# Optimization experiments

Hardware: AMD Instinct MI355X
Metric: run time of the kernel (lower is better)

The kernel has to match this reference:

```python
import jax, jax.numpy as jnp
import numpy as np

B, N, T = 2, 512, 4096
D_MODEL, N_MODES, NODE_H, EDGE_H = 128, 32, 128, 256


def _lin(key, d_in, d_out, scale=0.02):
    kw, kb = jax.random.split(key)
    W = jax.random.normal(kw, (d_in, d_out), jnp.float32) * scale
    b = jax.random.normal(kb, (d_out,), jnp.float32) * scale
    return W, b


def setup_inputs() -> dict:
    key = jax.random.key(0)
    ks = jax.random.split(key, 12)
    spikes = jax.random.normal(ks[0], (B, N, T), jnp.float32)
    # temporal FNO spectral weights (init * 0.01 as in torch)
    Wr = jax.random.normal(ks[1], (N_MODES, D_MODEL), jnp.float32) * 0.01
    Wi = jax.random.normal(ks[2], (N_MODES, D_MODEL), jnp.float32) * 0.01
    pw1, pb1 = _lin(ks[3], D_MODEL, D_MODEL)
    pw2, pb2 = _lin(ks[4], D_MODEL, D_MODEL)
    nw1, nb1 = _lin(ks[5], D_MODEL, NODE_H)
    nw2, nb2 = _lin(ks[6], NODE_H, D_MODEL)
    sw, sb = _lin(ks[7], D_MODEL, EDGE_H)
    tw, tb = _lin(ks[8], D_MODEL, EDGE_H)
    ew1, eb1 = _lin(ks[9], 2 * EDGE_H, EDGE_H)
    ew2, eb2 = _lin(ks[10], EDGE_H, EDGE_H // 2)
    ew3, eb3 = _lin(ks[11], EDGE_H // 2, 2)
    alpha = jnp.asarray(1.0, jnp.float32)
    beta = jnp.asarray(0.0, jnp.float32)
    return dict(spikes=spikes, Wr=Wr, Wi=Wi, pw1=pw1, pb1=pb1, pw2=pw2, pb2=pb2,
                nw1=nw1, nb1=nb1, nw2=nw2, nb2=nb2, sw=sw, sb=sb, tw=tw, tb=tb,
                ew1=ew1, eb1=eb1, ew2=ew2, eb2=eb2, ew3=ew3, eb3=eb3,
                alpha=alpha, beta=beta)


def reference(spikes, Wr, Wi, pw1, pb1, pw2, pb2, nw1, nb1, nw2, nb2,
              sw, sb, tw, tb, ew1, eb1, ew2, eb2, ew3, eb3, alpha, beta):
    relu = jax.nn.relu
    # --- TemporalFourierOperator1D ---
    xf = jnp.fft.rfft(spikes, axis=-1)[..., :N_MODES]          # [B,N,K] complex
    xr, xi = xf.real.astype(spikes.dtype), xf.imag.astype(spikes.dtype)
    # broadcast complex multiply: [B,N,K,1] x [K,D] -> [B,N,K,D]
    yr = xr[..., None] * Wr - xi[..., None] * Wi
    yi = xr[..., None] * Wi + xi[..., None] * Wr
    E = jnp.sqrt(yr * yr + yi * yi + 1e-8).mean(axis=2)         # [B,N,D]
    E = relu(E @ pw1 + pb1) @ pw2 + pb2                          # post_mlp
    # --- NodeFeatureNet ---
    H = relu(relu(E @ nw1 + nb1) @ nw2 + nb2)                    # [B,N,D]
    # --- EdgeFourierCoeffNet ---
    hs = H @ sw + sb                                             # [B,N,Eh]
    ht = H @ tw + tb
    # concat([hs,ht]) @ ew1 == hs @ ew1[:Eh] + ht @ ew1[Eh:] (exact same math)
    ps = hs @ ew1[:EDGE_H]                                       # [B,N,Eh]
    pt = ht @ ew1[EDGE_H:]
    h = relu(ps[:, :, None, :] + pt[:, None, :, :] + eb1)        # [B,N,N,Eh]
    h = relu(h @ ew2 + eb2)                                      # [B,N,N,Eh/2]
    rt = h @ ew3 + eb3                                           # [B,N,N,2]
    coeffs = rt[..., 0] + 1j * rt[..., 1]                        # [B,N,N] complex
    # --- AdjacencyLinearDecoder2D ---
    adj_spatial = jnp.fft.ifft2(coeffs, axes=(-2, -1)).real
    adj_logits = alpha * adj_spatial + beta
    adj_prob = jax.nn.sigmoid(adj_logits)
    return adj_logits, adj_prob
```

## Files before the change

### kernel.cpp

```cpp
#include <hip/hip_runtime.h>
#include <hip/hip_bf16.h>
#include <math.h>

typedef __attribute__((ext_vector_type(8))) short short8;
typedef __attribute__((ext_vector_type(8))) _Float16 f16x8;
typedef __attribute__((ext_vector_type(4))) float f32x4;

__device__ __forceinline__ short f2bf(float x) {
    union { float f; unsigned u; } v; v.f = x;
    unsigned r = v.u + 0x7fffu + ((v.u >> 16) & 1u);
    return (short)(r >> 16);
}
__device__ __forceinline__ unsigned cvtpk(float lo, float hi) {
    unsigned r;
    asm("v_cvt_pk_bf16_f32 %0, %1, %2" : "=v"(r) : "v"(lo), "v"(hi));
    return r;
}
__device__ __forceinline__ unsigned pk_addrelu(unsigned a, unsigned b) {
    unsigned r;
    asm("v_pk_add_f16 %0, %1, %2\n\tv_pk_max_f16 %0, %0, 0"
        : "=v"(r) : "v"(a), "v"(b));
    return r;
}
__device__ __forceinline__ float bflo(unsigned u) {
    union { unsigned u; float f; } v; v.u = u << 16; return v.f;
}
__device__ __forceinline__ float bfhi(unsigned u) {
    union { unsigned u; float f; } v; v.u = u & 0xffff0000u; return v.f;
}
union U32x4 { unsigned u[4]; short8 s8; };
union U32x4H { unsigned u[4]; f16x8 h8; };

__global__ __launch_bounds__(256) void setup_kernel(const float* __restrict__ ew2,
                                                    const float* __restrict__ pw1, const float* __restrict__ pw2,
                                                    const float* __restrict__ nw1, const float* __restrict__ nw2,
                                                    const float* __restrict__ sw, const float* __restrict__ tw,
                                                    const float* __restrict__ sb, const float* __restrict__ tb,
                                                    const float* __restrict__ ew1, const float* __restrict__ eb1,
                                                    short* __restrict__ W4P, short* __restrict__ F1P,
                                                    short* __restrict__ F2, _Float16* __restrict__ EW2H,
                                                    short* __restrict__ PWP,
                                                    short* __restrict__ WCP, float* __restrict__ BC) {
    __shared__ float2 tab[4096];
    __shared__ float eL2[256][32];
    int blk = blockIdx.x, tid = threadIdx.x;
    if (blk < 32) {
        for (int i = tid; i < 4096; i += 256) {
            float sn, cs; sincospif((float)i * (1.0f / 2048.0f), &sn, &cs);
            tab[i] = make_float2(cs, sn);
        }
        __syncthreads();
        int base = blk * 8192;
        #pragma unroll 4
        for (int u = 0; u < 32; ++u) {
            int i = base + u * 256 + tid;
            int j = i & 7, lane = (i >> 3) & 63, nf = (i >> 9) & 3, kkg = i >> 11;
            int k = kkg * 32 + (lane >> 4) * 8 + j;
            int n = nf * 16 + (lane & 15);
            float2 cs = tab[(k * (n & 31)) & 4095];
            W4P[i] = f2bf(n < 32 ? cs.x : -cs.y);
        }
    } else if (blk < 160) {
        for (int i = tid; i < 512; i += 256) {
            float sn, cs; sincospif((float)i * (1.0f / 256.0f), &sn, &cs);
            tab[i] = make_float2(cs, sn);
        }
        __syncthreads();
        int base = (blk - 32) * 8192;
        #pragma unroll 4
        for (int u = 0; u < 32; ++u) {
            int ii = base + u * 256 + tid;
            int j = ii & 7, lane = (ii >> 3) & 63, nfg = (ii >> 9) & 63, kk = ii >> 15;
            int k2 = kk * 32 + (lane >> 4) * 8 + j;
            int t = k2 >> 1, c = k2 & 1;
            int n = nfg * 16 + (lane & 15);
            int q = n >> 1, d = n & 1;
            float2 cs = tab[(t * q) & 511];
            F1P[ii] = f2bf((c == d) ? cs.x : (c ? -cs.y : cs.y));
        }
    } else if (blk < 224) {
        for (int i = tid; i < 512; i += 256) {
            float sn, cs; sincospif((float)i * (1.0f / 256.0f), &sn, &cs);
            tab[i] = make_float2(cs, sn);
        }
        __syncthreads();
        int base = (blk - 160) * 8192;
        #pragma unroll 4
        for (int u = 0; u < 32; ++u) {
            int ii = base + u * 256 + tid;
            int p = ii >> 10, k2 = ii & 1023;
            int s = k2 >> 1, dd = k2 & 1;
            float2 cs = tab[(p * s) & 511];
            F2[ii] = f2bf(dd ? -cs.y : cs.x);
        }
    } else if (blk < 236) {
        int base = (blk - 224) * 8192;
        #pragma unroll 4
        for (int u = 0; u < 32; ++u) {
            int ii = base + u * 256 + tid;
            if (ii < 32768) {
                int j = ii & 7, lane = (ii >> 3) & 63, hf = (ii >> 9) & 7, kk = ii >> 12;
                int k = kk * 32 + (lane >> 4) * 8 + j;
                int h = hf * 16 + (lane & 15);
                EW2H[ii] = (_Float16)ew2[k * 128 + h];
            } else {
                int iw = ii - 32768;
                int l = iw >> 14;
                int r = iw & 16383;
                int j = r & 7, lane = (r >> 3) & 63, nf = (r >> 9) & 7, kk = r >> 12;
                int k = kk * 32 + (lane >> 4) * 8 + j;
                int n = nf * 16 + (lane & 15);
                const float* W = (l == 0) ? pw1 : (l == 1) ? pw2 : (l == 2) ? nw1 : nw2;
                PWP[iw] = f2bf(W[k * 128 + n]);
            }
        }
    } else {
        int blk2 = blk - 236;
        int half = blk2 >> 3, jt = blk2 & 7, j0 = jt * 32;
        const float* ebase = ew1 + (size_t)half * 256 * 256;
        for (int it = 0; it < 32; ++it) {
            int idx = tid + it * 256;
            int i = idx >> 5, jj = idx & 31;
            eL2[i][jj] = ebase[(size_t)i * 256 + j0 + jj];
        }
        __syncthreads();
        const float* wp = half ? tw : sw;
        int d = tid >> 1, jh = tid & 1;
        float acc[16];
        #pragma unroll
        for (int x = 0; x < 16; ++x) acc[x] = 0.f;
        #pragma unroll 4
        for (int i = 0; i < 256; ++i) {
            float wv = wp[(size_t)d * 256 + i];
            #pragma unroll
            for (int x = 0; x < 16; ++x) acc[x] += wv * eL2[i][jh * 16 + x];
        }
        int kk = d >> 5, lg = (d >> 3) & 3, j = d & 7;
        #pragma unroll
        for (int x = 0; x < 16; ++x) {
            int n = half * 256 + j0 + jh * 16 + x;
            int lane = lg * 16 + (n & 15);
            WCP[((kk * 32 + (n >> 4)) * 64 + lane) * 8 + j] = f2bf(acc[x]);
        }
        if (tid < 32) {
            const float* bv = half ? tb : sb;
            float a = 0.f;
            #pragma unroll 8
            for (int i = 0; i < 256; ++i) a += bv[i] * eL2[i][tid];
            if (half == 0) a += eb1[j0 + tid];
            BC[half * 256 + j0 + tid] = a;
        }
    }
}

__global__ __launch_bounds__(256) void dft_mfma(const float* __restrict__ spikes,
                                                const short* __restrict__ W4P,
                                                float* __restrict__ X64P) {
    __shared__ float red[4][4][64][4];
    int part = blockIdx.x & 7;
    int row0 = (blockIdx.x >> 3) * 16;
    int tid = threadIdx.x, wid = tid >> 6, lane = tid & 63;
    int lrow = lane & 15, lg = lane >> 4;

    f32x4 acc[4];
    #pragma unroll
    for (int n = 0; n < 4; ++n) acc[n] = (f32x4){0.f, 0.f, 0.f, 0.f};

    int row = row0 + lrow;
    const float* sbase = spikes + (size_t)row * 4096;
    #pragma unroll
    for (int kk = 0; kk < 4; ++kk) {
        int k = part * 512 + wid * 128 + kk * 32 + lg * 8;
        const float4* sp = (const float4*)(sbase + k);
        float4 v0 = sp[0], v1 = sp[1];
        U32x4 a;
        a.u[0] = cvtpk(v0.x, v0.y);
        a.u[1] = cvtpk(v0.z, v0.w);
        a.u[2] = cvtpk(v1.x, v1.y);
        a.u[3] = cvtpk(v1.z, v1.w);
        int kkg = part * 16 + wid * 4 + kk;
        #pragma unroll
        for (int n = 0; n < 4; ++n) {
            short8 bfr = *(const short8*)(W4P + ((kkg * 4 + n) * 64 + lane) * 8);
            acc[n] = __builtin_amdgcn_mfma_f32_16x16x32_bf16(a.s8, bfr, acc[n], 0, 0, 0);
        }
    }
    #pragma unroll
    for (int n = 0; n < 4; ++n)
        #pragma unroll
        for (int r = 0; r < 4; ++r) red[wid][n][lane][r] = acc[n][r];
    __syncthreads();
    #pragma unroll
    for (int r = 0; r < 4; ++r) {
        float s = red[0][wid][lane][r] + red[1][wid][lane][r]
                + red[2][wid][lane][r] + red[3][wid][lane][r];
        int orow = row0 + lg * 4 + r;
        X64P[(size_t)part * 65536 + (size_t)orow * 64 + wid * 16 + lrow] = s;
    }
}

__global__ __launch_bounds__(512) void k_node(const float* __restrict__ X64P,
                                              const float* __restrict__ Wr, const float* __restrict__ Wi,
                                              const short* __restrict__ PWP,
                                              const float* __restrict__ pb1, const float* __restrict__ pb2,
                                              const float* __restrict__ nb1, const float* __restrict__ nb2,
                                              const short* __restrict__ WCP, const float* __restrict__ BC,
                                              _Float16* __restrict__ PS16, _Float16* __restrict__ PT16) {
    __shared__ float sx[16][64];
    __shared__ float wri[8192];
    __shared__ short abuf[16 * 128];
    int r0 = blockIdx.x * 16, tid = threadIdx.x;
    int wid = tid >> 6, lane = tid & 63;
    int lrow = lane & 15, lg = lane >> 4;

    #pragma unroll
    for (int it = 0; it < 2; ++it) {
        int idx = tid + it * 512;
        int row = idx >> 6, col = idx & 63;
        float v = 0.f;
        #pragma unroll
        for (int p = 0; p < 8; ++p)
            v += X64P[(size_t)p * 65536 + (size_t)(r0 + row) * 64 + col];
        sx[row][col] = v;
    }
    #pragma unroll
    for (int it = 0; it < 16; ++it) {
        int idx = tid + it * 512;
        wri[idx] = (idx < 4096) ? Wr[idx] : Wi[idx - 4096];
    }
    __syncthreads();

    #pragma unroll
    for (int it = 0; it < 4; ++it) {
        int idx = tid + it * 512;
        int row = idx >> 7, d = idx & 127;
        float acc = 0.f;
        #pragma unroll 8
        for (int k = 0; k < 32; ++k) {
            float a = sx[row][k], b = sx[row][32 + k];
            float wr = wri[k * 128 + d], wi = wri[4096 + k * 128 + d];
            float yr = a * wr - b * wi;
            float yi = a * wi + b * wr;
            acc += sqrtf(yr * yr + yi * yi + 1e-8f);
        }
        abuf[row * 128 + (d ^ ((row & 7) << 3))] = f2bf(acc * (1.0f / 32.0f));
    }
    __syncthreads();

    int asw = (lrow & 7) << 3;
    #pragma unroll 1
    for (int l = 0; l < 4; ++l) {
        f32x4 acc2 = (f32x4){0.f, 0.f, 0.f, 0.f};
        #pragma unroll
        for (int kk = 0; kk < 4; ++kk) {
            short8 a = *(const short8*)(abuf + lrow * 128 + ((kk * 32 + lg * 8) ^ asw));
            short8 b = *(const short8*)(PWP + (((l * 4 + kk) * 8 + wid) * 64 + lane) * 8);
            acc2 = __builtin_amdgcn_mfma_f32_16x16x32_bf16(a, b, acc2, 0, 0, 0);
        }
        __syncthreads();
        const float* bp = (l == 0) ? pb1 : (l == 1) ? pb2 : (l == 2) ? nb1 : nb2;
        bool rl = (l != 1);
        int n = wid * 16 + lrow;
        float bv = bp[n];
        #pragma unroll
        for (int r = 0; r < 4; ++r) {
            int orow = lg * 4 + r;
            float v = acc2[r] + bv;
            if (rl) v = fmaxf(v, 0.f);
            abuf[orow * 128 + (n ^ ((orow & 7) << 3))] = f2bf(v);
        }
        __syncthreads();
    }

    f32x4 acc3[4];
    #pragma unroll
    for (int f = 0; f < 4; ++f) acc3[f] = (f32x4){0.f, 0.f, 0.f, 0.f};
    #pragma unroll
    for (int kk = 0; kk < 4; ++kk) {
        short8 a = *(const short8*)(abuf + lrow * 128 + ((kk * 32 + lg * 8) ^ asw));
        #pragma unroll
        for (int f = 0; f < 4; ++f) {
            short8 b = *(const short8*)(WCP + ((kk * 32 + wid * 4 + f) * 64 + lane) * 8);
            acc3[f] = __builtin_amdgcn_mfma_f32_16x16x32_bf16(a, b, acc3[f], 0, 0, 0);
        }
    }
    #pragma unroll
    for (int f = 0; f < 4; ++f) {
        int n = (wid * 4 + f) * 16 + lrow;
        float bv = BC[n];
        _Float16* dst = (n < 256) ? (PS16 + n) : (PT16 + (n - 256));
        #pragma unroll
        for (int r = 0; r < 4; ++r) {
            int row = r0 + lg * 4 + r;
            dst[(size_t)row * 256] = (_Float16)(acc3[f][r] + bv);
        }
    }
}

__global__ __launch_bounds__(512, 2) void edge_mfma6(
    const unsigned* __restrict__ PS16, const unsigned* __restrict__ PT16,
    const uint4* __restrict__ EW2H4,
    const float* __restrict__ eb2, const float* __restrict__ ew3,
    const float* __restrict__ eb3, unsigned* __restrict__ CCP) {
    __shared__ __align__(16) unsigned pts[8192];
    __shared__ __align__(16) unsigned pss[2048];
    __shared__ float eb2s[64];
    __shared__ float ew3s[128];

    int bidx = blockIdx.x;
    int ttile = bidx & 7;
    int stile = (bidx >> 3) & 31;
    int b = (bidx >> 8) & 1;
    int hh = bidx >> 9;
    int s0 = stile * 16, t0 = ttile * 64;
    int tid = threadIdx.x;

    { const uint4* src = (const uint4*)(PT16 + (size_t)(b * 512 + t0) * 128);
      uint4* dst = (uint4*)pts;
      #pragma unroll
      for (int it = 0; it < 4; ++it) {
          int idx = tid + it * 512;
          int t = idx >> 5, g = idx & 31;
          dst[t * 32 + (g ^ (t & 7))] = src[idx];
      } }
    { const uint4* src = (const uint4*)(PS16 + (size_t)(b * 512 + s0) * 128);
      ((uint4*)pss)[tid] = src[tid]; }
    if (tid < 64) eb2s[tid] = eb2[hh * 64 + tid];
    if (tid < 128) ew3s[tid] = ew3[hh * 128 + tid];
    __syncthreads();

    int wid = tid >> 6, lane = tid & 63;
    int lrow = lane & 15, lg = lane >> 4;
    float e30 = hh ? 0.f : eb3[0];
    float e31 = hh ? 0.f : eb3[1];
    const uint4* pts4 = (const uint4*)pts;
    const uint4* pss4 = (const uint4*)pss;
    const uint4* ew2g = EW2H4 + hh * 256 + lane;

    #pragma unroll 1
    for (int i = 0; i < 2; ++i) {
        int s_local = wid * 2 + i;

        f32x4 acc[4][4];
        #pragma unroll
        for (int hf = 0; hf < 4; ++hf)
            #pragma unroll
            for (int tf = 0; tf < 4; ++tf) acc[hf][tf] = (f32x4){0.f, 0.f, 0.f, 0.f};

        #pragma unroll
        for (int kk = 0; kk < 8; ++kk) {
            uint4 pA = pss4[s_local * 32 + kk * 4 + lg];
            uint4 av0 = ew2g[kk * 512];
            uint4 av1 = ew2g[kk * 512 + 64];
            uint4 av2 = ew2g[kk * 512 + 128];
            uint4 av3 = ew2g[kk * 512 + 192];
            f16x8 bf[4];
            #pragma unroll
            for (int tf = 0; tf < 4; ++tf) {
                int t = tf * 16 + lrow;
                uint4 v = pts4[t * 32 + ((kk * 4 + lg) ^ (t & 7))];
                U32x4H r;
                r.u[0] = pk_addrelu(v.x, pA.x);
                r.u[1] = pk_addrelu(v.y, pA.y);
                r.u[2] = pk_addrelu(v.z, pA.z);
                r.u[3] = pk_addrelu(v.w, pA.w);
                bf[tf] = r.h8;
            }
            __builtin_amdgcn_s_setprio(1);
            #pragma unroll
            for (int hf = 0; hf < 4; ++hf) {
                U32x4H af;
                uint4 av = (hf == 0) ? av0 : (hf == 1) ? av1 : (hf == 2) ? av2 : av3;
                af.u[0] = av.x; af.u[1] = av.y; af.u[2] = av.z; af.u[3] = av.w;
                #pragma unroll
                for (int tf = 0; tf < 4; ++tf)
                    acc[hf][tf] = __builtin_amdgcn_mfma_f32_16x16x32_f16(af.h8, bf[tf], acc[hf][tf], 0, 0, 0);
            }
            __builtin_amdgcn_s_setprio(0);
        }

        size_t outbase = (size_t)hh * 524288 + (size_t)(b * 512 + s0 + s_local) * 512;
        #pragma unroll
        for (int tf = 0; tf < 4; ++tf) {
            float a0 = 0.f, a1 = 0.f;
            #pragma unroll
            for (int hf = 0; hf < 4; ++hf)
                #pragma unroll
                for (int r = 0; r < 4; ++r) {
                    int hl = hf * 16 + lg * 4 + r;
                    float hv = fmaxf(acc[hf][tf][r] + eb2s[hl], 0.f);
                    a0 += hv * ew3s[2 * hl];
                    a1 += hv * ew3s[2 * hl + 1];
                }
            a0 += __shfl_xor(a0, 16); a1 += __shfl_xor(a1, 16);
            a0 += __shfl_xor(a0, 32); a1 += __shfl_xor(a1, 32);
            if (lg == 0)
                CCP[outbase + t0 + tf * 16 + lrow] = cvtpk(a0 + e30, a1 + e31);
        }
    }
}

__global__ __launch_bounds__(256) void ifft1_mfma(const unsigned* __restrict__ CCP,
                                                  const short* __restrict__ F1P,
                                                  short* __restrict__ B2P) {
    __shared__ short st[32 * 64];
    int bidx = blockIdx.x;
    int nt = bidx & 7;
    int mt = bidx >> 3;
    int bs0 = mt * 16;
    int b = mt >> 5;
    int kk2 = mt & 31;
    int tid = threadIdx.x, wid = tid >> 6, lane = tid & 63;
    int lrow = lane & 15, lg = lane >> 4;

    f32x4 acc[2];
    acc[0] = (f32x4){0.f, 0.f, 0.f, 0.f};
    acc[1] = (f32x4){0.f, 0.f, 0.f, 0.f};

    const unsigned* r0p = CCP + (size_t)(bs0 + lrow) * 512 + lg * 4;
    const unsigned* r1p = r0p + 524288;
    #pragma unroll 4
    for (int kk = 0; kk < 32; ++kk) {
        uint4 x0 = *(const uint4*)(r0p + kk * 16);
        uint4 x1 = *(const uint4*)(r1p + kk * 16);
        U32x4 m;
        m.u[0] = cvtpk(bflo(x0.x) + bflo(x1.x), bfhi(x0.x) + bfhi(x1.x));
        m.u[1] = cvtpk(bflo(x0.y) + bflo(x1.y), bfhi(x0.y) + bfhi(x1.y));
        m.u[2] = cvtpk(bflo(x0.z) + bflo(x1.z), bfhi(x0.z) + bfhi(x1.z));
        m.u[3] = cvtpk(bflo(x0.w) + bflo(x1.w), bfhi(x0.w) + bfhi(x1.w));
        #pragma unroll
        for (int f = 0; f < 2; ++f) {
            int nfg = nt * 8 + wid * 2 + f;
            short8 bfr = *(const short8*)(F1P + ((kk * 64 + nfg) * 64 + lane) * 8);
            acc[f] = __builtin_amdgcn_mfma_f32_16x16x32_bf16(m.s8, bfr, acc[f], 0, 0, 0);
        }
    }
    #pragma unroll
    for (int f = 0; f < 2; ++f)
        #pragma unroll
        for (int r = 0; r < 4; ++r) {
            int n_local = (wid * 2 + f) * 16 + lrow;
            int lq = n_local >> 1, d = n_local & 1;
            int lk = (lg * 4 + r) * 2 + d;
            st[lk * 64 + lq] = f2bf(acc[f][r]);
        }
    __syncthreads();
    {
        int f2 = wid;
        int nf2 = nt * 4 + f2;
        short8 v;
        #pragma unroll
        for (int j = 0; j < 8; ++j)
            v[j] = st[((lane >> 4) * 8 + j) * 64 + f2 * 16 + (lane & 15)];
        *(short8*)(B2P + (size_t)b * 524288 + ((size_t)(kk2 * 32 + nf2) * 64 + lane) * 8) = v;
    }
}

__global__ __launch_bounds__(256) void ifft2_mfma(const short* __restrict__ B2P,
                                                  const short* __restrict__ F2,
                                                  const float* __restrict__ alpha, const float* __restrict__ beta,
                                                  float* __restrict__ out) {
    int bidx = blockIdx.x;
    int pt_ = bidx & 31;
    int qt = (bidx >> 5) & 7;
    int b = bidx >> 8;
    int p0 = pt_ * 16;
    int tid = threadIdx.x, wid = tid >> 6, lane = tid & 63;
    int lrow = lane & 15, lg = lane >> 4;

    f32x4 acc = (f32x4){0.f, 0.f, 0.f, 0.f};

    const short* arow = F2 + (size_t)(p0 + lrow) * 1024 + lg * 8;
    const short* bbase = B2P + (size_t)b * 524288;
    int nfg = qt * 4 + wid;
    #pragma unroll 4
    for (int kk = 0; kk < 32; ++kk) {
        short8 a = *(const short8*)(arow + kk * 32);
        short8 bfr = *(const short8*)(bbase + ((size_t)(kk * 32 + nfg) * 64 + lane) * 8);
        acc = __builtin_amdgcn_mfma_f32_16x16x32_bf16(a, bfr, acc, 0, 0, 0);
    }
    float al = alpha[0], be = beta[0];
    const float scale = 1.0f / (512.0f * 512.0f);
    #pragma unroll
    for (int r = 0; r < 4; ++r) {
        int q = qt * 64 + wid * 16 + lrow;
        int p = p0 + lg * 4 + r;
        float l = al * (acc[r] * scale) + be;
        size_t idx = (size_t)b * 262144 + (size_t)p * 512 + q;
        out[idx] = l;
        out[524288 + idx] = 1.f / (1.f + expf(-l));
    }
}

extern "C" void kernel_launch(void* const* d_in, const int* in_sizes, int n_in,
                              void* d_out, int out_size, void* d_ws, size_t ws_size,
                              hipStream_t stream) {
    const float* spikes = (const float*)d_in[0];
    const float* Wr  = (const float*)d_in[1];
    const float* Wi  = (const float*)d_in[2];
    const float* pw1 = (const float*)d_in[3];
    const float* pb1 = (const float*)d_in[4];
    const float* pw2 = (const float*)d_in[5];
    const float* pb2 = (const float*)d_in[6];
    const float* nw1 = (const float*)d_in[7];
    const float* nb1 = (const float*)d_in[8];
    const float* nw2 = (const float*)d_in[9];
    const float* nb2 = (const float*)d_in[10];
    const float* sw  = (const float*)d_in[11];
    const float* sb  = (const float*)d_in[12];
    const float* tw_ = (const float*)d_in[13];
    const float* tb  = (const float*)d_in[14];
    const float* ew1 = (const float*)d_in[15];
    const float* eb1 = (const float*)d_in[16];
    const float* ew2 = (const float*)d_in[17];
    const float* eb2 = (const float*)d_in[18];
    const float* ew3 = (const float*)d_in[19];
    const float* eb3 = (const float*)d_in[20];
    const float* alpha = (const float*)d_in[21];
    const float* beta  = (const float*)d_in[22];
    float* out = (float*)d_out;
    float* ws  = (float*)d_ws;

    unsigned* CCP   = (unsigned*)(ws + 0);
    float*    X64P  = ws + 0;
    short*    WCP   = (short*)(ws + 524288);
    float*    BC    = ws + 557056;
    _Float16* PS16  = (_Float16*)(ws + 1048576);
    _Float16* PT16  = (_Float16*)(ws + 1179648);
    short*    B2P   = (short*)(ws + 1048576);
    _Float16* EW2H  = (_Float16*)(ws + 1572864);
    short*    W4P   = (short*)(ws + 1589248);
    short*    F1P   = (short*)(ws + 1720320);
    short*    F2    = (short*)(ws + 2244608);
    short*    PWP   = (short*)(ws + 2506752);

    setup_kernel<<<252, 256, 0, stream>>>(ew2, pw1, pw2, nw1, nw2, sw, tw_, sb, tb, ew1, eb1,
                                          W4P, F1P, F2, EW2H, PWP, WCP, BC);
    dft_mfma<<<512, 256, 0, stream>>>(spikes, W4P, X64P);
    k_node<<<64, 512, 0, stream>>>(X64P, Wr, Wi, PWP, pb1, pb2, nb1, nb2, WCP, BC, PS16, PT16);
    edge_mfma6<<<1024, 512, 0, stream>>>((const unsigned*)PS16, (const unsigned*)PT16,
                                         (const uint4*)EW2H, eb2, ew3, eb3, CCP);
    ifft1_mfma<<<512, 256, 0, stream>>>(CCP, F1P, B2P);
    ifft2_mfma<<<512, 256, 0, stream>>>(B2P, F2, alpha, beta, out);
}
```

Baseline: 124.5 us.

## Merge edge hidden-half split into one block, drop partial-sum combine in ifft1

```diff
diff --git a/kernel.cpp b/kernel.cpp
--- a/kernel.cpp
+++ b/kernel.cpp
@@ -21,12 +21,6 @@
     asm("v_pk_add_f16 %0, %1, %2\n\tv_pk_max_f16 %0, %0, 0"
         : "=v"(r) : "v"(a), "v"(b));
     return r;
-}
-__device__ __forceinline__ float bflo(unsigned u) {
-    union { unsigned u; float f; } v; v.u = u << 16; return v.f;
-}
-__device__ __forceinline__ float bfhi(unsigned u) {
-    union { unsigned u; float f; } v; v.u = u & 0xffff0000u; return v.f;
 }
 union U32x4 { unsigned u[4]; short8 s8; };
 union U32x4H { unsigned u[4]; f16x8 h8; };
@@ -297,21 +291,20 @@
     }
 }
 
-__global__ __launch_bounds__(512, 2) void edge_mfma6(
+__global__ __launch_bounds__(512, 2) void edge_mfma7(
     const unsigned* __restrict__ PS16, const unsigned* __restrict__ PT16,
     const uint4* __restrict__ EW2H4,
     const float* __restrict__ eb2, const float* __restrict__ ew3,
-    const float* __restrict__ eb3, unsigned* __restrict__ CCP) {
+    const float* __restrict__ eb3, unsigned* __restrict__ CC32) {
     __shared__ __align__(16) unsigned pts[8192];
     __shared__ __align__(16) unsigned pss[2048];
-    __shared__ float eb2s[64];
-    __shared__ float ew3s[128];
+    __shared__ float eb2s[128];
+    __shared__ float ew3s[256];
 
     int bidx = blockIdx.x;
     int ttile = bidx & 7;
     int stile = (bidx >> 3) & 31;
-    int b = (bidx >> 8) & 1;
-    int hh = bidx >> 9;
+    int b = bidx >> 8;
     int s0 = stile * 16, t0 = ttile * 64;
     int tid = threadIdx.x;
 
@@ -325,82 +318,83 @@
       } }
     { const uint4* src = (const uint4*)(PS16 + (size_t)(b * 512 + s0) * 128);
       ((uint4*)pss)[tid] = src[tid]; }
-    if (tid < 64) eb2s[tid] = eb2[hh * 64 + tid];
-    if (tid < 128) ew3s[tid] = ew3[hh * 128 + tid];
+    if (tid < 128) eb2s[tid] = eb2[tid];
+    if (tid < 256) ew3s[tid] = ew3[tid];
     __syncthreads();
 
     int wid = tid >> 6, lane = tid & 63;
     int lrow = lane & 15, lg = lane >> 4;
-    float e30 = hh ? 0.f : eb3[0];
-    float e31 = hh ? 0.f : eb3[1];
+    float e30 = eb3[0], e31 = eb3[1];
     const uint4* pts4 = (const uint4*)pts;
     const uint4* pss4 = (const uint4*)pss;
-    const uint4* ew2g = EW2H4 + hh * 256 + lane;
+    const uint4* ew2g = EW2H4 + lane;
 
     #pragma unroll 1
     for (int i = 0; i < 2; ++i) {
         int s_local = wid * 2 + i;
-
-        f32x4 acc[4][4];
-        #pragma unroll
-        for (int hf = 0; hf < 4; ++hf)
+        #pragma unroll 1
+        for (int tp = 0; tp < 2; ++tp) {
+            f32x4 acc[8][2];
             #pragma unroll
-            for (int tf = 0; tf < 4; ++tf) acc[hf][tf] = (f32x4){0.f, 0.f, 0.f, 0.f};
-
-        #pragma unroll
-        for (int kk = 0; kk < 8; ++kk) {
-            uint4 pA = pss4[s_local * 32 + kk * 4 + lg];
-            uint4 av0 = ew2g[kk * 512];
-            uint4 av1 = ew2g[kk * 512 + 64];
-            uint4 av2 = ew2g[kk * 512 + 128];
-            uint4 av3 = ew2g[kk * 512 + 192];
-            f16x8 bf[4];
+            for (int hf = 0; hf < 8; ++hf)
+                #pragma unroll
+                for (int tf = 0; tf < 2; ++tf) acc[hf][tf] = (f32x4){0.f, 0.f, 0.f, 0.f};
+
             #pragma unroll
-            for (int tf = 0; tf < 4; ++tf) {
-                int t = tf * 16 + lrow;
-                uint4 v = pts4[t * 32 + ((kk * 4 + lg) ^ (t & 7))];
-                U32x4H r;
-                r.u[0] = pk_addrelu(v.x, pA.x);
-                r.u[1] = pk_addrelu(v.y, pA.y);
-                r.u[2] = pk_addrelu(v.z, pA.z);
-                r.u[3] = pk_addrelu(v.w, pA.w);
-                bf[tf] = r.h8;
+            for (int kk = 0; kk < 8; ++kk) {
+                uint4 pA = pss4[s_local * 32 + kk * 4 + lg];
+                f16x8 bf[2];
+                #pragma unroll
+                for (int tf = 0; tf < 2; ++tf) {
+                    int t = tp * 32 + tf * 16 + lrow;
+                    uint4 v = pts4[t * 32 + ((kk * 4 + lg) ^ (t & 7))];
+                    U32x4H r;
+                    r.u[0] = pk_addrelu(v.x, pA.x);
+                    r.u[1] = pk_addrelu(v.y, pA.y);
+                    r.u[2] = pk_addrelu(v.z, pA.z);
+                    r.u[3] = pk_addrelu(v.w, pA.w);
+                    bf[tf] = r.h8;
+                }
+                __builtin_amdgcn_s_setprio(1);
+                #pragma unroll
+                for (int hfp = 0; hfp < 4; ++hfp) {
+                    uint4 ava = ew2g[(kk * 8 + 2 * hfp) * 64];
+                    uint4 avb = ew2g[(kk * 8 + 2 * hfp + 1) * 64];
+                    U32x4H afa, afb;
+                    afa.u[0] = ava.x; afa.u[1] = ava.y; afa.u[2] = ava.z; afa.u[3] = ava.w;
+                    afb.u[0] = avb.x; afb.u[1] = avb.y; afb.u[2] = avb.z; afb.u[3] = avb.w;
+                    #pragma unroll
+                    for (int tf = 0; tf < 2; ++tf) {
+                        acc[2 * hfp][tf]     = __builtin_amdgcn_mfma_f32_16x16x32_f16(afa.h8, bf[tf], acc[2 * hfp][tf], 0, 0, 0);
+                        acc[2 * hfp + 1][tf] = __builtin_amdgcn_mfma_f32_16x16x32_f16(afb.h8, bf[tf], acc[2 * hfp + 1][tf], 0, 0, 0);
+                    }
+                }
+                __builtin_amdgcn_s_setprio(0);
             }
-            __builtin_amdgcn_s_setprio(1);
+
+            size_t outrow = (size_t)(b * 512 + s0 + s_local) * 512;
             #pragma unroll
-            for (int hf = 0; hf < 4; ++hf) {
-                U32x4H af;
-                uint4 av = (hf == 0) ? av0 : (hf == 1) ? av1 : (hf == 2) ? av2 : av3;
-                af.u[0] = av.x; af.u[1] = av.y; af.u[2] = av.z; af.u[3] = av.w;
+            for (int tf = 0; tf < 2; ++tf) {
+                float a0 = 0.f, a1 = 0.f;
                 #pragma unroll
-                for (int tf = 0; tf < 4; ++tf)
-                    acc[hf][tf] = __builtin_amdgcn_mfma_f32_16x16x32_f16(af.h8, bf[tf], acc[hf][tf], 0, 0, 0);
+                for (int hf = 0; hf < 8; ++hf)
+                    #pragma unroll
+                    for (int r = 0; r < 4; ++r) {
+                        int h = hf * 16 + lg * 4 + r;
+                        float hv = fmaxf(acc[hf][tf][r] + eb2s[h], 0.f);
+                        a0 += hv * ew3s[2 * h];
+                        a1 += hv * ew3s[2 * h + 1];
+                    }
+                a0 += __shfl_xor(a0, 16); a1 += __shfl_xor(a1, 16);
+                a0 += __shfl_xor(a0, 32); a1 += __shfl_xor(a1, 32);
+                if (lg == 0)
+                    CC32[outrow + t0 + tp * 32 + tf * 16 + lrow] = cvtpk(a0 + e30, a1 + e31);
             }
-            __builtin_amdgcn_s_setprio(0);
-        }
-
-        size_t outbase = (size_t)hh * 524288 + (size_t)(b * 512 + s0 + s_local) * 512;
-        #pragma unroll
-        for (int tf = 0; tf < 4; ++tf) {
-            float a0 = 0.f, a1 = 0.f;
-            #pragma unroll
-            for (int hf = 0; hf < 4; ++hf)
-                #pragma unroll
-                for (int r = 0; r < 4; ++r) {
-                    int hl = hf * 16 + lg * 4 + r;
-                    float hv = fmaxf(acc[hf][tf][r] + eb2s[hl], 0.f);
-                    a0 += hv * ew3s[2 * hl];
-                    a1 += hv * ew3s[2 * hl + 1];
-                }
-            a0 += __shfl_xor(a0, 16); a1 += __shfl_xor(a1, 16);
-            a0 += __shfl_xor(a0, 32); a1 += __shfl_xor(a1, 32);
-            if (lg == 0)
-                CCP[outbase + t0 + tf * 16 + lrow] = cvtpk(a0 + e30, a1 + e31);
-        }
-    }
-}
-
-__global__ __launch_bounds__(256) void ifft1_mfma(const unsigned* __restrict__ CCP,
+        }
+    }
+}
+
+__global__ __launch_bounds__(256) void ifft1_mfma(const short* __restrict__ CC,
                                                   const short* __restrict__ F1P,
                                                   short* __restrict__ B2P) {
     __shared__ short st[32 * 64];
@@ -417,22 +411,15 @@
     acc[0] = (f32x4){0.f, 0.f, 0.f, 0.f};
     acc[1] = (f32x4){0.f, 0.f, 0.f, 0.f};
 
-    const unsigned* r0p = CCP + (size_t)(bs0 + lrow) * 512 + lg * 4;
-    const unsigned* r1p = r0p + 524288;
+    const short* arow = CC + (size_t)(bs0 + lrow) * 1024 + lg * 8;
     #pragma unroll 4
     for (int kk = 0; kk < 32; ++kk) {
-        uint4 x0 = *(const uint4*)(r0p + kk * 16);
-        uint4 x1 = *(const uint4*)(r1p + kk * 16);
-        U32x4 m;
-        m.u[0] = cvtpk(bflo(x0.x) + bflo(x1.x), bfhi(x0.x) + bfhi(x1.x));
-        m.u[1] = cvtpk(bflo(x0.y) + bflo(x1.y), bfhi(x0.y) + bfhi(x1.y));
-        m.u[2] = cvtpk(bflo(x0.z) + bflo(x1.z), bfhi(x0.z) + bfhi(x1.z));
-        m.u[3] = cvtpk(bflo(x0.w) + bflo(x1.w), bfhi(x0.w) + bfhi(x1.w));
+        short8 a = *(const short8*)(arow + kk * 32);
         #pragma unroll
         for (int f = 0; f < 2; ++f) {
             int nfg = nt * 8 + wid * 2 + f;
             short8 bfr = *(const short8*)(F1P + ((kk * 64 + nfg) * 64 + lane) * 8);
-            acc[f] = __builtin_amdgcn_mfma_f32_16x16x32_bf16(m.s8, bfr, acc[f], 0, 0, 0);
+            acc[f] = __builtin_amdgcn_mfma_f32_16x16x32_bf16(a, bfr, acc[f], 0, 0, 0);
         }
     }
     #pragma unroll
@@ -521,7 +508,7 @@
     float* out = (float*)d_out;
     float* ws  = (float*)d_ws;
 
-    unsigned* CCP   = (unsigned*)(ws + 0);
+    unsigned* CC    = (unsigned*)(ws + 0);
     float*    X64P  = ws + 0;
     short*    WCP   = (short*)(ws + 524288);
     float*    BC    = ws + 557056;
@@ -538,8 +525,8 @@
                                           W4P, F1P, F2, EW2H, PWP, WCP, BC);
     dft_mfma<<<512, 256, 0, stream>>>(spikes, W4P, X64P);
     k_node<<<64, 512, 0, stream>>>(X64P, Wr, Wi, PWP, pb1, pb2, nb1, nb2, WCP, BC, PS16, PT16);
-    edge_mfma6<<<1024, 512, 0, stream>>>((const unsigned*)PS16, (const unsigned*)PT16,
-                                         (const uint4*)EW2H, eb2, ew3, eb3, CCP);
-    ifft1_mfma<<<512, 256, 0, stream>>>(CCP, F1P, B2P);
+    edge_mfma7<<<512, 512, 0, stream>>>((const unsigned*)PS16, (const unsigned*)PT16,
+                                        (const uint4*)EW2H, eb2, ew3, eb3, CC);
+    ifft1_mfma<<<512, 256, 0, stream>>>((const short*)CC, F1P, B2P);
     ifft2_mfma<<<512, 256, 0, stream>>>(B2P, F2, alpha, beta, out);
 }
```

After: 139.1 us. 11.8% more time.
